# Optimization experiments

Hardware: AMD Instinct MI355X
Metric: run time of the kernel (lower is better)

Reference implementation:

```python
import jax, jax.numpy as jnp
import numpy as np

B, N, DQ, DK, DV = 8, 2048, 1024, 1024, 1024

def setup_inputs() -> dict:
    key = jax.random.key(0)
    kx, kq, kk, kv = jax.random.split(key, 4)
    x = jax.random.normal(kx, (B, N, DQ), dtype=jnp.float32)
    # nn.Linear(dim_q, dim_k, bias=False) weights: [out, in]
    s = 1.0 / np.sqrt(DQ)
    Wq = jax.random.uniform(kq, (DK, DQ), jnp.float32, -s, s)
    Wk = jax.random.uniform(kk, (DK, DQ), jnp.float32, -s, s)
    Wv = jax.random.uniform(kv, (DV, DQ), jnp.float32, -s, s)
    return {"x": x, "Wq": Wq, "Wk": Wk, "Wv": Wv}

def reference(x, Wq, Wk, Wv):
    batch, n, _ = x.shape
    q = jnp.einsum('bnd,kd->bnk', x, Wq)  # [B,n,DK]
    k = jnp.einsum('bnd,kd->bnk', x, Wk)  # [B,n,DK]
    v = jnp.einsum('bnd,vd->bnv', x, Wv)  # [B,n,DV]
    norm = 1.0 / jnp.sqrt(jnp.asarray(Wq.shape[0], jnp.float32))
    dist = jnp.einsum('bik,bjk->bij', q, k) * norm  # [B,n,n]
    causal = jnp.tril(jnp.ones((n, n), dtype=bool))
    dist = jnp.where(causal[None, :, :], dist, jnp.float32(-1e20))
    dist = jax.nn.softmax(dist, axis=-1)
    att = jnp.einsum('bij,bjv->biv', dist, v)  # [B,n,DV]
    return att
```

## Files before the change

### kernel.cpp

```cpp
#include <hip/hip_runtime.h>
#include <hip/hip_bf16.h>

#define BM 128
#define BN 128
#define BK 32
#define TILE_ELEMS (BM * BK)

typedef __attribute__((ext_vector_type(4))) float floatx4;
typedef __bf16 bf16x8 __attribute__((ext_vector_type(8)));
typedef unsigned int u32;
typedef unsigned short u16;

typedef __attribute__((address_space(1))) const u32 g_u32;
typedef __attribute__((address_space(3))) u32 l_u32;

__device__ __forceinline__ u16 f32_to_bf16(float f) {
    union { float f; u32 u; } x{f};
    u32 u = x.u;
    u32 r = (u + 0x7fffu + ((u >> 16) & 1u)) >> 16;
    return (u16)r;
}


__device__ __forceinline__ void stage_half_sw(const u16* gbase, u16* lds_half, int tid) {
    int lane = tid & 63;
    int rsub = lane >> 3;
    int colsw = ((lane & 7) ^ rsub) << 3;
#pragma unroll
    for (int j = 0; j < 2; ++j) {
        int q = (tid >> 6) * 2 + j;
        int row = q * 8 + rsub;
        const u16* g = gbase + row * 1024 + colsw;
        u16* l = lds_half + q * 512 + lane * 8;
        __builtin_amdgcn_global_load_lds((g_u32*)g, (l_u32*)l, 16, 0, 0);
    }
}

__global__ __launch_bounds__(512, 2)
void qkv_gemm8(const u16* __restrict__ A, const u16* __restrict__ Bw,
               u16* __restrict__ QKi, u16* __restrict__ Vt)
{
    __shared__ u16 As[2][256 * 64];
    __shared__ u16 Bs[2][256 * 64];

    int bid = blockIdx.x;
    int wg = (bid & 7) * 96 + (bid >> 3);
    int mt = wg / 12, nt = wg - mt * 12;

    int tid = threadIdx.x;
    int lane = tid & 63, wv = tid >> 6;
    int wr = wv >> 2, wc = wv & 3;
    int lrow = lane & 15, quad = lane >> 4;
    int sw = lrow & 7;

    const u16* Ab = A + (long)mt * 256 * 1024;
    const u16* Bb = Bw + (long)nt * 256 * 1024;

    stage_half_sw(Bb,                  &Bs[0][0],        tid);
    stage_half_sw(Bb + 128 * 1024,     &Bs[0][128 * 64], tid);
    stage_half_sw(Ab,                  &As[0][0],        tid);
    stage_half_sw(Ab + 128 * 1024,     &As[0][128 * 64], tid);
    stage_half_sw(Bb + 64,             &Bs[1][0],        tid);
    stage_half_sw(Bb + 64 + 128 * 1024,&Bs[1][128 * 64], tid);
    asm volatile("s_waitcnt vmcnt(4)" ::: "memory");
    __builtin_amdgcn_sched_barrier(0);
    __builtin_amdgcn_s_barrier();

    floatx4 acc[8][4] = {};

    const int arow = (wr * 128 + lrow) * 64;
    const int brow = (wc * 64 + lrow) * 64;
    const int sl0 = (quad ^ sw) * 8;
    const int sl1 = ((4 + quad) ^ sw) * 8;

    for (int i = 0; i < 8; ++i) {
        int t1  = 2 * i + 1;
        int tn  = (2 * i + 2 <= 15) ? 2 * i + 2 : 15;
        int tn1 = (2 * i + 3 <= 15) ? 2 * i + 3 : 15;
        const u16* gA1 = Ab + t1 * 64;
        const u16* gB2 = Bb + tn * 64;
        const u16* gA2 = Ab + tn * 64;
        const u16* gB3 = Bb + tn1 * 64;

        bf16x8 bq0[4], bq1[4];
#pragma unroll
        for (int half = 0; half < 2; ++half) {
#pragma unroll
            for (int p = 0; p < 4; ++p) {
                if (p == 0) {
#pragma unroll
                    for (int ni = 0; ni < 4; ++ni) {
                        bq0[ni] = *(const bf16x8*)&Bs[half][brow + ni * 1024 + sl0];
                        bq1[ni] = *(const bf16x8*)&Bs[half][brow + ni * 1024 + sl1];
                    }
                }
                bf16x8 a00 = *(const bf16x8*)&As[half][arow + (2 * p)     * 1024 + sl0];
                bf16x8 a01 = *(const bf16x8*)&As[half][arow + (2 * p)     * 1024 + sl1];
                bf16x8 a10 = *(const bf16x8*)&As[half][arow + (2 * p + 1) * 1024 + sl0];
                bf16x8 a11 = *(const bf16x8*)&As[half][arow + (2 * p + 1) * 1024 + sl1];

                int ph = half * 4 + p;
                switch (ph) {
                    case 0: stage_half_sw(gA1,              &As[1][0],        tid); break;
                    case 1: stage_half_sw(gA1 + 128 * 1024, &As[1][128 * 64], tid); break;
                    case 2: stage_half_sw(gB2,              &Bs[0][0],        tid); break;
                    case 3: stage_half_sw(gB2 + 128 * 1024, &Bs[0][128 * 64], tid); break;
                    case 4: stage_half_sw(gA2,              &As[0][0],        tid); break;
                    case 5: stage_half_sw(gA2 + 128 * 1024, &As[0][128 * 64], tid); break;
                    case 6: stage_half_sw(gB3,              &Bs[1][0],        tid); break;
                    case 7: stage_half_sw(gB3 + 128 * 1024, &Bs[1][128 * 64], tid); break;
                }

                __builtin_amdgcn_s_barrier();
                __builtin_amdgcn_s_setprio(1);
                int m0 = 2 * p;
#pragma unroll
                for (int ni = 0; ni < 4; ++ni) {
                    acc[m0][ni]     = __builtin_amdgcn_mfma_f32_16x16x32_bf16(a00, bq0[ni], acc[m0][ni],     0, 0, 0);
                    acc[m0][ni]     = __builtin_amdgcn_mfma_f32_16x16x32_bf16(a01, bq1[ni], acc[m0][ni],     0, 0, 0);
                    acc[m0 + 1][ni] = __builtin_amdgcn_mfma_f32_16x16x32_bf16(a10, bq0[ni], acc[m0 + 1][ni], 0, 0, 0);
                    acc[m0 + 1][ni] = __builtin_amdgcn_mfma_f32_16x16x32_bf16(a11, bq1[ni], acc[m0 + 1][ni], 0, 0, 0);
                }
                __builtin_amdgcn_s_setprio(0);
                if (p == 3) {
                    asm volatile("s_waitcnt vmcnt(4)" ::: "memory");
                    __builtin_amdgcn_sched_barrier(0);
                }
                __builtin_amdgcn_s_barrier();
            }
        }
    }
    asm volatile("s_waitcnt vmcnt(0)" ::: "memory");
    __builtin_amdgcn_sched_barrier(0);

    if (nt < 8) {
        long crow0 = (long)mt * 256 + wr * 128 + quad * 4;
        int  ccol0 = nt * 256 + wc * 64 + lrow;
#pragma unroll
        for (int mi = 0; mi < 8; ++mi) {
#pragma unroll
            for (int r = 0; r < 4; ++r) {
                long row = crow0 + mi * 16 + r;
#pragma unroll
                for (int ni = 0; ni < 4; ++ni)
                    QKi[row * 2048 + ccol0 + ni * 16] = f32_to_bf16(acc[mi][ni][r]);
            }
        }
    } else {
        int dv0   = (nt - 8) * 256 + wc * 64 + lrow;
        long tok0 = (long)mt * 256 + wr * 128 + quad * 4;
#pragma unroll
        for (int mi = 0; mi < 8; ++mi) {
#pragma unroll
            for (int ni = 0; ni < 4; ++ni) {
                ushort4 o;
                o.x = f32_to_bf16(acc[mi][ni][0]);
                o.y = f32_to_bf16(acc[mi][ni][1]);
                o.z = f32_to_bf16(acc[mi][ni][2]);
                o.w = f32_to_bf16(acc[mi][ni][3]);
                *(ushort4*)(Vt + (long)(dv0 + ni * 16) * 16384 + tok0 + mi * 16) = o;
            }
        }
    }
}


__device__ __forceinline__ void stage_tile(const u16* gbase, int ld, u16* lds, int tid) {
#pragma unroll
    for (int it = 0; it < 2; ++it) {
        int flat = it * 2048 + tid * 8;
        int row = flat >> 5;
        int col = flat & 31;
        const u16* g = gbase + (long)row * ld + col;
        __builtin_amdgcn_global_load_lds((g_u32*)g, (l_u32*)(&lds[flat]), 16, 0, 0);
    }
}

template<bool OUT_BF16, int MODE>
__device__ __forceinline__ void gemm_body(
    const u16* __restrict__ Ab, const u16* __restrict__ Bb, void* __restrict__ Cb,
    int lda, int ldb, long ldc, int m0, int n0, int nkt, float scale,
    u16* As, u16* Bs, float* lsum)
{
    int tid = threadIdx.x;

    const u16* Arow = Ab + (long)m0 * lda;
    const u16* Brow = Bb + (long)n0 * ldb;

    stage_tile(Arow, lda, As, tid);
    stage_tile(Brow, ldb, Bs, tid);

    int wave = tid >> 6, lane = tid & 63;
    int wr = (wave >> 1) * 64, wc = (wave & 1) * 64;
    int lrow = lane & 15, quad = lane >> 4;

    floatx4 acc[4][4] = {};
    const int aoff = (wr + lrow) * BK + quad * 8;
    const int boff = (wc + lrow) * BK + quad * 8;

    for (int kt = 0; kt < nkt; ++kt) {
        __syncthreads();
        bf16x8 af[4], bfr[4];
#pragma unroll
        for (int i = 0; i < 4; ++i) {
            af[i]  = *(const bf16x8*)&As[aoff + i * 16 * BK];
            bfr[i] = *(const bf16x8*)&Bs[boff + i * 16 * BK];
        }
#pragma unroll
        for (int mi = 0; mi < 4; ++mi)
#pragma unroll
            for (int ni = 0; ni < 4; ++ni)
                acc[mi][ni] = __builtin_amdgcn_mfma_f32_16x16x32_bf16(af[mi], bfr[ni], acc[mi][ni], 0, 0, 0);
        __syncthreads();
        if (kt + 1 < nkt) {
            stage_tile(Arow + (kt + 1) * BK, lda, As, tid);
            stage_tile(Brow + (kt + 1) * BK, ldb, Bs, tid);
        }
    }

    long crow0 = m0 + wr + quad * 4;
    int  ccol0 = n0 + wc + lrow;
#pragma unroll
    for (int mi = 0; mi < 4; ++mi) {
#pragma unroll
        for (int r = 0; r < 4; ++r) {
            long row = crow0 + mi * 16 + r;
            float rs = 0.f;
#pragma unroll
            for (int ni = 0; ni < 4; ++ni) {
                long col = ccol0 + ni * 16;
                float v = acc[mi][ni][r] * scale;
                if (MODE == 1) {
                    float e = (col > row) ? 0.f : __expf(v);
                    ((u16*)Cb)[row * ldc + col] = f32_to_bf16(e);
                    rs += e;
                } else {
                    if (OUT_BF16) ((u16*)Cb)[row * ldc + col] = f32_to_bf16(v);
                    else          ((float*)Cb)[row * ldc + col] = v;
                }
            }
            if (MODE == 1) {
                rs += __shfl_xor(rs, 1, 16);
                rs += __shfl_xor(rs, 2, 16);
                rs += __shfl_xor(rs, 4, 16);
                rs += __shfl_xor(rs, 8, 16);
                if (lrow == 0) atomicAdd(&lsum[row], rs);
            }
        }
    }
}

__global__ __launch_bounds__(256)
void s_gemm(const u16* __restrict__ QKi, u16* __restrict__ P, float* __restrict__ lsum)
{
    __shared__ u16 As[TILE_ELEMS];
    __shared__ u16 Bs[TILE_ELEMS];
    int b = blockIdx.x, u = blockIdx.y, v = blockIdx.z;
    int mt, nt;
    if (u <= v) { mt = v; nt = u; } else { mt = 15 - v; nt = u - v - 1; }
    const u16* Ab = QKi + (long)b * 2048 * 2048;
    const u16* Bb = Ab + 1024;
    gemm_body<true, 1>(Ab, Bb, P + (long)b * 2048 * 2048, 2048, 2048, 2048,
                       mt * BM, nt * BN, 32, 0.03125f, As, Bs, lsum + b * 2048);
}

__global__ __launch_bounds__(512)
void pv_gemm2(const u16* __restrict__ P, const u16* __restrict__ Vt,
              float* __restrict__ O, const float* __restrict__ lsum)
{
    __shared__ u16 As[128 * 32];
    __shared__ u16 Bs[256 * 32];
    int b = blockIdx.x, nt = blockIdx.y, mt = 15 - blockIdx.z;
    const u16* Ab = P  + (long)b * 2048 * 2048 + (long)mt * 128 * 2048;
    const u16* Bb = Vt + (long)b * 2048 + (long)nt * 256 * 16384;
    float* Ob = O + (long)b * 2048 * 1024;
    const float* ls = lsum + b * 2048;
    int nkt = mt * 4 + 4;

    int tid = threadIdx.x, lane = tid & 63, wave = tid >> 6;
    int wr = wave >> 2, wc = wave & 3;
    int lrow = lane & 15, quad = lane >> 4;

    {
        int flat = tid * 8, row = flat >> 5, col = flat & 31;
        __builtin_amdgcn_global_load_lds((g_u32*)(Ab + (long)row * 2048 + col),
                                         (l_u32*)&As[flat], 16, 0, 0);
#pragma unroll
        for (int it = 0; it < 2; ++it) {
            int f2 = it * 4096 + tid * 8, r2 = f2 >> 5, c2 = f2 & 31;
            __builtin_amdgcn_global_load_lds((g_u32*)(Bb + (long)r2 * 16384 + c2),
                                             (l_u32*)&Bs[f2], 16, 0, 0);
        }
    }

    floatx4 acc[4][4] = {};
    const int aoff = (wr * 64 + lrow) * 32 + quad * 8;
    const int boff = (wc * 64 + lrow) * 32 + quad * 8;

    for (int kt = 0; kt < nkt; ++kt) {
        __syncthreads();
        bf16x8 af[4], bfr[4];
#pragma unroll
        for (int i = 0; i < 4; ++i) {
            af[i]  = *(const bf16x8*)&As[aoff + i * 16 * 32];
            bfr[i] = *(const bf16x8*)&Bs[boff + i * 16 * 32];
        }
#pragma unroll
        for (int mi = 0; mi < 4; ++mi)
#pragma unroll
            for (int ni = 0; ni < 4; ++ni)
                acc[mi][ni] = __builtin_amdgcn_mfma_f32_16x16x32_bf16(af[mi], bfr[ni], acc[mi][ni], 0, 0, 0);
        __syncthreads();
        if (kt + 1 < nkt) {
            const u16* An = Ab + (kt + 1) * 32;
            const u16* Bn = Bb + (kt + 1) * 32;
            int flat = tid * 8, row = flat >> 5, col = flat & 31;
            __builtin_amdgcn_global_load_lds((g_u32*)(An + (long)row * 2048 + col),
                                             (l_u32*)&As[flat], 16, 0, 0);
#pragma unroll
            for (int it = 0; it < 2; ++it) {
                int f2 = it * 4096 + tid * 8, r2 = f2 >> 5, c2 = f2 & 31;
                __builtin_amdgcn_global_load_lds((g_u32*)(Bn + (long)r2 * 16384 + c2),
                                                 (l_u32*)&Bs[f2], 16, 0, 0);
            }
        }
    }

    int crow0 = mt * 128 + wr * 64 + quad * 4;
    int ccol0 = nt * 256 + wc * 64 + lrow;
#pragma unroll
    for (int mi = 0; mi < 4; ++mi) {
#pragma unroll
        for (int r = 0; r < 4; ++r) {
            int row = crow0 + mi * 16 + r;
            float linv = 1.0f / ls[row];
#pragma unroll
            for (int ni = 0; ni < 4; ++ni)
                Ob[(long)row * 1024 + ccol0 + ni * 16] = acc[mi][ni][r] * linv;
        }
    }
}

__global__ __launch_bounds__(256)
void cvt_f32_bf16(const float* __restrict__ src, u16* __restrict__ dst, long n)
{
    long idx = ((long)blockIdx.x * 256 + threadIdx.x) << 2;
    if (idx >= n) return;
    float4 f = *(const float4*)(src + idx);
    ushort4 o;
    o.x = f32_to_bf16(f.x); o.y = f32_to_bf16(f.y);
    o.z = f32_to_bf16(f.z); o.w = f32_to_bf16(f.w);
    *(ushort4*)(dst + idx) = o;
}

__global__ __launch_bounds__(256)
void cvt_w3(const float* __restrict__ Wq, const float* __restrict__ Wk,
            const float* __restrict__ Wv, u16* __restrict__ dst)
{
    int which = blockIdx.x >> 10;
    const float* src = which == 0 ? Wq : (which == 1 ? Wk : Wv);
    long base = (long)(blockIdx.x & 1023) * 1024 + threadIdx.x * 4;
    float4 f = *(const float4*)(src + base);
    ushort4 o;
    o.x = f32_to_bf16(f.x); o.y = f32_to_bf16(f.y);
    o.z = f32_to_bf16(f.z); o.w = f32_to_bf16(f.w);
    *(ushort4*)(dst + (long)which * 1048576 + base) = o;
}

extern "C" void kernel_launch(void* const* d_in, const int* in_sizes, int n_in,
                              void* d_out, int out_size, void* d_ws, size_t ws_size,
                              hipStream_t stream)
{
    const int B = 8, N = 2048, D = 1024;
    const long MT = (long)B * N;
    const long nX = MT * D;
    const long nW = (long)D * D;

    const float* x  = (const float*)d_in[0];
    const float* Wq = (const float*)d_in[1];
    const float* Wk = (const float*)d_in[2];
    const float* Wv = (const float*)d_in[3];
    float* out = (float*)d_out;

    u16* wb   = (u16*)d_ws;
    u16* xb   = wb + 3 * nW;
    u16* QKi  = xb + nX;
    u16* Vt   = QKi + MT * 2048;
    u16* P    = Vt + nX;
    float* lsum = (float*)wb;

    cvt_f32_bf16<<<(int)(nX / 1024), 256, 0, stream>>>(x, xb, nX);
    cvt_w3<<<3072, 256, 0, stream>>>(Wq, Wk, Wv, wb);

    qkv_gemm8<<<dim3(768, 1, 1), 512, 0, stream>>>(xb, wb, QKi, Vt);

    hipMemsetAsync(lsum, 0, (size_t)B * N * sizeof(float), stream);

    s_gemm<<<dim3(8, 17, 8), 256, 0, stream>>>(QKi, P, lsum);

    pv_gemm2<<<dim3(8, 4, 16), 512, 0, stream>>>(P, Vt, out, lsum);
}
```

Baseline: 361.1 us.

## Port QK^T score GEMM to the 256x256 eight-phase pipelined kernel

Turns the optimized 256x256 tile, eight-phase double-buffered GEMM main loop into a macro taking strides, and reuses it for the causal score GEMM in place of the simple 128x128 BK=32 kernel. Causal lower-triangle tiles are enumerated via a triangular index (36 tiles per batch, 288 blocks). The aim is better data reuse, swizzled LDS loads and load/compute overlap for the S=QK^T stage. The cost is that coarser 256 tiles on the diagonal compute more masked-out work, and there are fewer blocks to spread across CUs.

```diff
diff --git a/kernel.cpp b/kernel.cpp
--- a/kernel.cpp
+++ b/kernel.cpp
@@ -1,10 +1,5 @@
 #include <hip/hip_runtime.h>
 #include <hip/hip_bf16.h>
-
-#define BM 128
-#define BN 128
-#define BK 32
-#define TILE_ELEMS (BM * BK)
 
 typedef __attribute__((ext_vector_type(4))) float floatx4;
 typedef __bf16 bf16x8 __attribute__((ext_vector_type(8)));
@@ -22,7 +17,7 @@
 }
 
 
-__device__ __forceinline__ void stage_half_sw(const u16* gbase, u16* lds_half, int tid) {
+__device__ __forceinline__ void stage_half_sw(const u16* gbase, int ld, u16* lds_half, int tid) {
     int lane = tid & 63;
     int rsub = lane >> 3;
     int colsw = ((lane & 7) ^ rsub) << 3;
@@ -30,11 +25,78 @@
     for (int j = 0; j < 2; ++j) {
         int q = (tid >> 6) * 2 + j;
         int row = q * 8 + rsub;
-        const u16* g = gbase + row * 1024 + colsw;
+        const u16* g = gbase + (long)row * ld + colsw;
         u16* l = lds_half + q * 512 + lane * 8;
         __builtin_amdgcn_global_load_lds((g_u32*)g, (l_u32*)l, 16, 0, 0);
     }
 }
+
+#define EIGHT_PHASE_K1024_LOOP(Ab, Bb, lda, ldb)                                       \
+    stage_half_sw(Bb,                  ldb, &Bs[0][0],        tid);                    \
+    stage_half_sw(Bb + 128 * (ldb),    ldb, &Bs[0][128 * 64], tid);                    \
+    stage_half_sw(Ab,                  lda, &As[0][0],        tid);                    \
+    stage_half_sw(Ab + 128 * (lda),    lda, &As[0][128 * 64], tid);                    \
+    stage_half_sw(Bb + 64,             ldb, &Bs[1][0],        tid);                    \
+    stage_half_sw(Bb + 64 + 128 * (ldb), ldb, &Bs[1][128 * 64], tid);                  \
+    asm volatile("s_waitcnt vmcnt(4)" ::: "memory");                                   \
+    __builtin_amdgcn_sched_barrier(0);                                                 \
+    __builtin_amdgcn_s_barrier();                                                      \
+    for (int i = 0; i < 8; ++i) {                                                      \
+        int t1  = 2 * i + 1;                                                           \
+        int tn  = (2 * i + 2 <= 15) ? 2 * i + 2 : 15;                                  \
+        int tn1 = (2 * i + 3 <= 15) ? 2 * i + 3 : 15;                                  \
+        const u16* gA1 = Ab + t1 * 64;                                                 \
+        const u16* gB2 = Bb + tn * 64;                                                 \
+        const u16* gA2 = Ab + tn * 64;                                                 \
+        const u16* gB3 = Bb + tn1 * 64;                                                \
+        bf16x8 bq0[4], bq1[4];                                                         \
+        _Pragma("unroll")                                                              \
+        for (int half = 0; half < 2; ++half) {                                         \
+            _Pragma("unroll")                                                          \
+            for (int p = 0; p < 4; ++p) {                                              \
+                if (p == 0) {                                                          \
+                    _Pragma("unroll")                                                  \
+                    for (int ni = 0; ni < 4; ++ni) {                                   \
+                        bq0[ni] = *(const bf16x8*)&Bs[half][brow + ni * 1024 + sl0];   \
+                        bq1[ni] = *(const bf16x8*)&Bs[half][brow + ni * 1024 + sl1];   \
+                    }                                                                  \
+                }                                                                      \
+                bf16x8 a00 = *(const bf16x8*)&As[half][arow + (2 * p)     * 1024 + sl0]; \
+                bf16x8 a01 = *(const bf16x8*)&As[half][arow + (2 * p)     * 1024 + sl1]; \
+                bf16x8 a10 = *(const bf16x8*)&As[half][arow + (2 * p + 1) * 1024 + sl0]; \
+                bf16x8 a11 = *(const bf16x8*)&As[half][arow + (2 * p + 1) * 1024 + sl1]; \
+                int ph = half * 4 + p;                                                 \
+                switch (ph) {                                                          \
+                    case 0: stage_half_sw(gA1,              lda, &As[1][0],        tid); break; \
+                    case 1: stage_half_sw(gA1 + 128 * (lda), lda, &As[1][128 * 64], tid); break; \
+                    case 2: stage_half_sw(gB2,              ldb, &Bs[0][0],        tid); break; \
+                    case 3: stage_half_sw(gB2 + 128 * (ldb), ldb, &Bs[0][128 * 64], tid); break; \
+                    case 4: stage_half_sw(gA2,              lda, &As[0][0],        tid); break; \
+                    case 5: stage_half_sw(gA2 + 128 * (lda), lda, &As[0][128 * 64], tid); break; \
+                    case 6: stage_half_sw(gB3,              ldb, &Bs[1][0],        tid); break; \
+                    case 7: stage_half_sw(gB3 + 128 * (ldb), ldb, &Bs[1][128 * 64], tid); break; \
+                }                                                                      \
+                __builtin_amdgcn_s_barrier();                                          \
+                __builtin_amdgcn_s_setprio(1);                                         \
+                int m0 = 2 * p;                                                        \
+                _Pragma("unroll")                                                      \
+                for (int ni = 0; ni < 4; ++ni) {                                       \
+                    acc[m0][ni]     = __builtin_amdgcn_mfma_f32_16x16x32_bf16(a00, bq0[ni], acc[m0][ni],     0, 0, 0); \
+                    acc[m0][ni]     = __builtin_amdgcn_mfma_f32_16x16x32_bf16(a01, bq1[ni], acc[m0][ni],     0, 0, 0); \
+                    acc[m0 + 1][ni] = __builtin_amdgcn_mfma_f32_16x16x32_bf16(a10, bq0[ni], acc[m0 + 1][ni], 0, 0, 0); \
+                    acc[m0 + 1][ni] = __builtin_amdgcn_mfma_f32_16x16x32_bf16(a11, bq1[ni], acc[m0 + 1][ni], 0, 0, 0); \
+                }                                                                      \
+                __builtin_amdgcn_s_setprio(0);                                         \
+                if (p == 3) {                                                          \
+                    asm volatile("s_waitcnt vmcnt(4)" ::: "memory");                   \
+                    __builtin_amdgcn_sched_barrier(0);                                 \
+                }                                                                      \
+                __builtin_amdgcn_s_barrier();                                          \
+            }                                                                          \
+        }                                                                              \
+    }                                                                                  \
+    asm volatile("s_waitcnt vmcnt(0)" ::: "memory");                                   \
+    __builtin_amdgcn_sched_barrier(0);
 
 __global__ __launch_bounds__(512, 2)
 void qkv_gemm8(const u16* __restrict__ A, const u16* __restrict__ Bw,
@@ -56,82 +118,13 @@
     const u16* Ab = A + (long)mt * 256 * 1024;
     const u16* Bb = Bw + (long)nt * 256 * 1024;
 
-    stage_half_sw(Bb,                  &Bs[0][0],        tid);
-    stage_half_sw(Bb + 128 * 1024,     &Bs[0][128 * 64], tid);
-    stage_half_sw(Ab,                  &As[0][0],        tid);
-    stage_half_sw(Ab + 128 * 1024,     &As[0][128 * 64], tid);
-    stage_half_sw(Bb + 64,             &Bs[1][0],        tid);
-    stage_half_sw(Bb + 64 + 128 * 1024,&Bs[1][128 * 64], tid);
-    asm volatile("s_waitcnt vmcnt(4)" ::: "memory");
-    __builtin_amdgcn_sched_barrier(0);
-    __builtin_amdgcn_s_barrier();
-
     floatx4 acc[8][4] = {};
-
     const int arow = (wr * 128 + lrow) * 64;
     const int brow = (wc * 64 + lrow) * 64;
     const int sl0 = (quad ^ sw) * 8;
     const int sl1 = ((4 + quad) ^ sw) * 8;
 
-    for (int i = 0; i < 8; ++i) {
-        int t1  = 2 * i + 1;
-        int tn  = (2 * i + 2 <= 15) ? 2 * i + 2 : 15;
-        int tn1 = (2 * i + 3 <= 15) ? 2 * i + 3 : 15;
-        const u16* gA1 = Ab + t1 * 64;
-        const u16* gB2 = Bb + tn * 64;
-        const u16* gA2 = Ab + tn * 64;
-        const u16* gB3 = Bb + tn1 * 64;
-
-        bf16x8 bq0[4], bq1[4];
-#pragma unroll
-        for (int half = 0; half < 2; ++half) {
-#pragma unroll
-            for (int p = 0; p < 4; ++p) {
-                if (p == 0) {
-#pragma unroll
-                    for (int ni = 0; ni < 4; ++ni) {
-                        bq0[ni] = *(const bf16x8*)&Bs[half][brow + ni * 1024 + sl0];
-                        bq1[ni] = *(const bf16x8*)&Bs[half][brow + ni * 1024 + sl1];
-                    }
-                }
-                bf16x8 a00 = *(const bf16x8*)&As[half][arow + (2 * p)     * 1024 + sl0];
-                bf16x8 a01 = *(const bf16x8*)&As[half][arow + (2 * p)     * 1024 + sl1];
-                bf16x8 a10 = *(const bf16x8*)&As[half][arow + (2 * p + 1) * 1024 + sl0];
-                bf16x8 a11 = *(const bf16x8*)&As[half][arow + (2 * p + 1) * 1024 + sl1];
-
-                int ph = half * 4 + p;
-                switch (ph) {
-                    case 0: stage_half_sw(gA1,              &As[1][0],        tid); break;
-                    case 1: stage_half_sw(gA1 + 128 * 1024, &As[1][128 * 64], tid); break;
-                    case 2: stage_half_sw(gB2,              &Bs[0][0],        tid); break;
-                    case 3: stage_half_sw(gB2 + 128 * 1024, &Bs[0][128 * 64], tid); break;
-                    case 4: stage_half_sw(gA2,              &As[0][0],        tid); break;
-                    case 5: stage_half_sw(gA2 + 128 * 1024, &As[0][128 * 64], tid); break;
-                    case 6: stage_half_sw(gB3,              &Bs[1][0],        tid); break;
-                    case 7: stage_half_sw(gB3 + 128 * 1024, &Bs[1][128 * 64], tid); break;
-                }
-
-                __builtin_amdgcn_s_barrier();
-                __builtin_amdgcn_s_setprio(1);
-                int m0 = 2 * p;
-#pragma unroll
-                for (int ni = 0; ni < 4; ++ni) {
-                    acc[m0][ni]     = __builtin_amdgcn_mfma_f32_16x16x32_bf16(a00, bq0[ni], acc[m0][ni],     0, 0, 0);
-                    acc[m0][ni]     = __builtin_amdgcn_mfma_f32_16x16x32_bf16(a01, bq1[ni], acc[m0][ni],     0, 0, 0);
-                    acc[m0 + 1][ni] = __builtin_amdgcn_mfma_f32_16x16x32_bf16(a10, bq0[ni], acc[m0 + 1][ni], 0, 0, 0);
-                    acc[m0 + 1][ni] = __builtin_amdgcn_mfma_f32_16x16x32_bf16(a11, bq1[ni], acc[m0 + 1][ni], 0, 0, 0);
-                }
-                __builtin_amdgcn_s_setprio(0);
-                if (p == 3) {
-                    asm volatile("s_waitcnt vmcnt(4)" ::: "memory");
-                    __builtin_amdgcn_sched_barrier(0);
-                }
-                __builtin_amdgcn_s_barrier();
-            }
-        }
-    }
-    asm volatile("s_waitcnt vmcnt(0)" ::: "memory");
-    __builtin_amdgcn_sched_barrier(0);
+    EIGHT_PHASE_K1024_LOOP(Ab, Bb, 1024, 1024)
 
     if (nt < 8) {
         long crow0 = (long)mt * 256 + wr * 128 + quad * 4;
@@ -164,104 +157,62 @@
     }
 }
 
-
-__device__ __forceinline__ void stage_tile(const u16* gbase, int ld, u16* lds, int tid) {
-#pragma unroll
-    for (int it = 0; it < 2; ++it) {
-        int flat = it * 2048 + tid * 8;
-        int row = flat >> 5;
-        int col = flat & 31;
-        const u16* g = gbase + (long)row * ld + col;
-        __builtin_amdgcn_global_load_lds((g_u32*)g, (l_u32*)(&lds[flat]), 16, 0, 0);
-    }
-}
-
-template<bool OUT_BF16, int MODE>
-__device__ __forceinline__ void gemm_body(
-    const u16* __restrict__ Ab, const u16* __restrict__ Bb, void* __restrict__ Cb,
-    int lda, int ldb, long ldc, int m0, int n0, int nkt, float scale,
-    u16* As, u16* Bs, float* lsum)
-{
+__global__ __launch_bounds__(512, 2)
+void s_gemm8(const u16* __restrict__ QKi, u16* __restrict__ P, float* __restrict__ lsum)
+{
+    __shared__ u16 As[2][256 * 64];
+    __shared__ u16 Bs[2][256 * 64];
+
+    int bid = blockIdx.x;
+    int b  = bid & 7;
+    int ti = bid >> 3;
+    int mt = (int)((__builtin_sqrtf(8.0f * ti + 1.0f) - 1.0f) * 0.5f);
+    while ((mt + 1) * (mt + 2) / 2 <= ti) ++mt;
+    while (mt * (mt + 1) / 2 > ti) --mt;
+    int nt = ti - mt * (mt + 1) / 2;
+
     int tid = threadIdx.x;
-
-    const u16* Arow = Ab + (long)m0 * lda;
-    const u16* Brow = Bb + (long)n0 * ldb;
-
-    stage_tile(Arow, lda, As, tid);
-    stage_tile(Brow, ldb, Bs, tid);
-
-    int wave = tid >> 6, lane = tid & 63;
-    int wr = (wave >> 1) * 64, wc = (wave & 1) * 64;
+    int lane = tid & 63, wv = tid >> 6;
+    int wr = wv >> 2, wc = wv & 3;
     int lrow = lane & 15, quad = lane >> 4;
-
-    floatx4 acc[4][4] = {};
-    const int aoff = (wr + lrow) * BK + quad * 8;
-    const int boff = (wc + lrow) * BK + quad * 8;
-
-    for (int kt = 0; kt < nkt; ++kt) {
-        __syncthreads();
-        bf16x8 af[4], bfr[4];
-#pragma unroll
-        for (int i = 0; i < 4; ++i) {
-            af[i]  = *(const bf16x8*)&As[aoff + i * 16 * BK];
-            bfr[i] = *(const bf16x8*)&Bs[boff + i * 16 * BK];
-        }
-#pragma unroll
-        for (int mi = 0; mi < 4; ++mi)
-#pragma unroll
-            for (int ni = 0; ni < 4; ++ni)
-                acc[mi][ni] = __builtin_amdgcn_mfma_f32_16x16x32_bf16(af[mi], bfr[ni], acc[mi][ni], 0, 0, 0);
-        __syncthreads();
-        if (kt + 1 < nkt) {
-            stage_tile(Arow + (kt + 1) * BK, lda, As, tid);
-            stage_tile(Brow + (kt + 1) * BK, ldb, Bs, tid);
-        }
-    }
-
-    long crow0 = m0 + wr + quad * 4;
-    int  ccol0 = n0 + wc + lrow;
-#pragma unroll
-    for (int mi = 0; mi < 4; ++mi) {
+    int sw = lrow & 7;
+
+    const u16* Qb = QKi + (long)b * 2048 * 2048 + (long)mt * 256 * 2048;
+    const u16* Kb = QKi + (long)b * 2048 * 2048 + (long)nt * 256 * 2048 + 1024;
+    u16* Pb = P + (long)b * 2048 * 2048;
+    float* ls = lsum + b * 2048;
+
+    floatx4 acc[8][4] = {};
+    const int arow = (wr * 128 + lrow) * 64;
+    const int brow = (wc * 64 + lrow) * 64;
+    const int sl0 = (quad ^ sw) * 8;
+    const int sl1 = ((4 + quad) ^ sw) * 8;
+
+    EIGHT_PHASE_K1024_LOOP(Qb, Kb, 2048, 2048)
+
+    int crow0 = mt * 256 + wr * 128 + quad * 4;
+    int ccol0 = nt * 256 + wc * 64 + lrow;
+#pragma unroll
+    for (int mi = 0; mi < 8; ++mi) {
 #pragma unroll
         for (int r = 0; r < 4; ++r) {
-            long row = crow0 + mi * 16 + r;
+            int row = crow0 + mi * 16 + r;
             float rs = 0.f;
 #pragma unroll
             for (int ni = 0; ni < 4; ++ni) {
-                long col = ccol0 + ni * 16;
-                float v = acc[mi][ni][r] * scale;
-                if (MODE == 1) {
-                    float e = (col > row) ? 0.f : __expf(v);
-                    ((u16*)Cb)[row * ldc + col] = f32_to_bf16(e);
-                    rs += e;
-                } else {
-                    if (OUT_BF16) ((u16*)Cb)[row * ldc + col] = f32_to_bf16(v);
-                    else          ((float*)Cb)[row * ldc + col] = v;
-                }
+                int col = ccol0 + ni * 16;
+                float v = acc[mi][ni][r] * 0.03125f;
+                float e = (col > row) ? 0.f : __expf(v);
+                Pb[(long)row * 2048 + col] = f32_to_bf16(e);
+                rs += e;
             }
-            if (MODE == 1) {
-                rs += __shfl_xor(rs, 1, 16);
-                rs += __shfl_xor(rs, 2, 16);
-                rs += __shfl_xor(rs, 4, 16);
-                rs += __shfl_xor(rs, 8, 16);
-                if (lrow == 0) atomicAdd(&lsum[row], rs);
-            }
-        }
-    }
-}
-
-__global__ __launch_bounds__(256)
-void s_gemm(const u16* __restrict__ QKi, u16* __restrict__ P, float* __restrict__ lsum)
-{
-    __shared__ u16 As[TILE_ELEMS];
-    __shared__ u16 Bs[TILE_ELEMS];
-    int b = blockIdx.x, u = blockIdx.y, v = blockIdx.z;
-    int mt, nt;
-    if (u <= v) { mt = v; nt = u; } else { mt = 15 - v; nt = u - v - 1; }
-    const u16* Ab = QKi + (long)b * 2048 * 2048;
-    const u16* Bb = Ab + 1024;
-    gemm_body<true, 1>(Ab, Bb, P + (long)b * 2048 * 2048, 2048, 2048, 2048,
-                       mt * BM, nt * BN, 32, 0.03125f, As, Bs, lsum + b * 2048);
+            rs += __shfl_xor(rs, 1, 16);
+            rs += __shfl_xor(rs, 2, 16);
+            rs += __shfl_xor(rs, 4, 16);
+            rs += __shfl_xor(rs, 8, 16);
+            if (lrow == 0) atomicAdd(&ls[row], rs);
+        }
+    }
 }
 
 __global__ __launch_bounds__(512)
@@ -396,7 +347,7 @@
 
     hipMemsetAsync(lsum, 0, (size_t)B * N * sizeof(float), stream);
 
-    s_gemm<<<dim3(8, 17, 8), 256, 0, stream>>>(QKi, P, lsum);
+    s_gemm8<<<dim3(288, 1, 1), 512, 0, stream>>>(QKi, P, lsum);
 
     pv_gemm2<<<dim3(8, 4, 16), 512, 0, stream>>>(P, Vt, out, lsum);
 }
```

Result: no change. 362.2 us (+0.3%).
